# Kernel tuning notes

Measured on AMD Instinct MI355X. Metric: run time of the kernel, lower is better.

The kernel has to match this reference:

```python
import jax, jax.numpy as jnp
import numpy as np

GROUP1 = jnp.array([2, 3, 5, 6, 1, 4, 0, 7, 8, 9, 14, 15, 11, 12, 10, 13])
GROUP2 = jnp.array([0, 1, 2, 3, 5, 6, 4, 7])
NUM_HEADS = 8
LN_EPS = 1e-5


def setup_inputs() -> dict:
    key = jax.random.key(0)
    ks = jax.random.split(key, 4)
    B, N, C = 4096, 16, 512
    s = 1.0 / np.sqrt(C)
    return {
        "x": jax.random.normal(ks[0], (B, N, C), dtype=jnp.float32),
        "Wq": jax.random.normal(ks[1], (C, C), dtype=jnp.float32) * s,
        "Wkv": jax.random.normal(ks[2], (C, 2 * C), dtype=jnp.float32) * s,
        "Wproj": jax.random.normal(ks[3], (C, C), dtype=jnp.float32) * s,
        "bproj": jnp.zeros((C,), dtype=jnp.float32),
        "gamma": jnp.ones((C,), dtype=jnp.float32),
        "beta": jnp.zeros((C,), dtype=jnp.float32),
    }


def reference(x, Wq, Wkv, Wproj, bproj, gamma, beta):
    B, N, C = x.shape
    H = NUM_HEADS
    hd = C // H
    scale = hd ** -0.5

    # gather into fixed groups, avg-pool adjacent pairs along the joint axis
    p1 = x[:, GROUP1].reshape(B, 8, 2, C).mean(axis=2)   # [B, 8, C]
    p2 = x[:, GROUP2].reshape(B, 4, 2, C).mean(axis=2)   # [B, 4, C]
    pools = jnp.concatenate([x, p1, p2], axis=1)         # [B, 28, C]

    # LayerNorm over channel dim
    mu = pools.mean(axis=-1, keepdims=True)
    var = pools.var(axis=-1, keepdims=True)
    pools = (pools - mu) * jax.lax.rsqrt(var + LN_EPS) * gamma + beta

    q = (x @ Wq).reshape(B, N, H, hd)                    # [B, N, H, hd]
    kv = (pools @ Wkv).reshape(B, -1, 2, H, hd)          # [B, 28, 2, H, hd]
    k, v = kv[:, :, 0], kv[:, :, 1]                      # [B, 28, H, hd]

    attn = jnp.einsum("bnhd,bmhd->bhnm", q, k) * scale   # [B, H, N, 28]
    attn = jax.nn.softmax(attn, axis=-1)
    out = jnp.einsum("bhnm,bmhd->bnhd", attn, v).reshape(B, N, C)
    return out @ Wproj + bproj
```

## Files before the change

### kernel.cpp

```cpp
#include <hip/hip_runtime.h>

typedef unsigned short u16;
typedef __attribute__((ext_vector_type(8))) short s8v;
typedef __attribute__((ext_vector_type(4))) float f4v;

#define NB 4

__device__ __forceinline__ float bf2f(u16 u) {
    union { unsigned u; float f; } c; c.u = ((unsigned)u) << 16; return c.f;
}
__device__ __forceinline__ u16 f2bf(float f) {
    union { float f; unsigned u; } c; c.f = f;
    return (u16)((c.u + 0x7FFFu + ((c.u >> 16) & 1u)) >> 16);
}
__device__ __forceinline__ f4v mfma16(s8v a, s8v b, f4v c) {
    return __builtin_amdgcn_mfma_f32_16x16x32_bf16(a, b, c, 0, 0, 0);
}

__constant__ int POOL_A[12] = {2,5,1,0,8,14,11,10, 0,2,5,4};
__constant__ int POOL_B[12] = {3,6,4,7,9,15,12,13, 1,3,6,7};

__global__ void pack_wcat(const float* __restrict__ Wq, const float* __restrict__ Wkv,
                          const float* __restrict__ gamma, u16* __restrict__ Wfrag) {
    int blk = blockIdx.x;
    int kt = blk & 15, hn = blk >> 4;
    int nt = hn % 12, h = hn / 12;
    int lane = threadIdx.x, l15 = lane & 15, quad = lane >> 4;
    int r0 = kt * 32 + quad * 8;
    s8v v;
    if (nt < 4) {
        int c = h * 64 + nt * 16 + l15;
#pragma unroll
        for (int j = 0; j < 8; ++j) v[j] = (short)f2bf(Wq[(size_t)(r0 + j) * 512 + c]);
    } else {
        int c = (nt < 8) ? (h * 64 + (nt - 4) * 16 + l15)
                         : (512 + h * 64 + (nt - 8) * 16 + l15);
#pragma unroll
        for (int j = 0; j < 8; ++j)
            v[j] = (short)f2bf(gamma[r0 + j] * Wkv[(size_t)(r0 + j) * 1024 + c]);
    }
    *(s8v*)&Wfrag[(size_t)blk * 512 + lane * 8] = v;
}

__global__ void pack_wp(const float* __restrict__ Wproj, u16* __restrict__ Wpfrag) {
    int blk = blockIdx.x;
    int n = blk & 31, hk = blk >> 5;
    int kt = hk & 1, h = hk >> 1;
    int lane = threadIdx.x, l15 = lane & 15, quad = lane >> 4;
    int r0 = h * 64 + kt * 32 + quad * 8;
    int c = n * 16 + l15;
    s8v v;
#pragma unroll
    for (int j = 0; j < 8; ++j) v[j] = (short)f2bf(Wproj[(size_t)(r0 + j) * 512 + c]);
    *(s8v*)&Wpfrag[(size_t)blk * 512 + lane * 8] = v;
}

__global__ void gemv_g(const float* __restrict__ Wkv, const float* __restrict__ gamma,
                       const float* __restrict__ beta, float* __restrict__ gkv) {
    __shared__ float red[256];
    int o = blockIdx.x * 64 + (threadIdx.x & 63);
    int rc = threadIdx.x >> 6;
    int h = o >> 8, s = (o >> 6) & 3, c = o & 63;
    int col = (s < 2) ? (h * 64 + c) : (512 + h * 64 + c);
    const float* vec = (s & 1) ? beta : gamma;
    float acc = 0.f;
    for (int r = rc * 128; r < rc * 128 + 128; ++r)
        acc += vec[r] * Wkv[(size_t)r * 1024 + col];
    red[threadIdx.x] = acc;
    __syncthreads();
    if (rc == 0)
        gkv[o] = red[threadIdx.x] + red[threadIdx.x + 64] +
                 red[threadIdx.x + 128] + red[threadIdx.x + 192];
}

__global__ __launch_bounds__(1024, 4) void fused_spa(
    const float* __restrict__ x,
    const u16*  __restrict__ Wfrag,
    const u16*  __restrict__ Wpfrag,
    const float* __restrict__ gkv,
    const float* __restrict__ bproj,
    float* __restrict__ out)
{
    __shared__ __align__(16) unsigned char smem[162816];
    u16*   XS   = (u16*)smem;
    float* YS   = (float*)(smem + 66560);
    u16*   QH   = (u16*)(smem + 100352);
    u16*   OS   = (u16*)(smem + 109568);
    u16*   KH   = (u16*)(smem + 118784);
    u16*   VT   = (u16*)(smem + 137216);
    u16*   PB   = (u16*)(smem + 157696);
    float* STraw   = (float*)(smem + 161792);
    float* STcross = (float*)(smem + 162304);
    float* STfin   = (float*)(smem + 161792);

    const int tid  = (int)threadIdx.x;
    const int w    = tid >> 6;
    const int lane = tid & 63;
    const int l15  = lane & 15;
    const int quad = lane >> 4;
    const size_t grow0 = (size_t)blockIdx.x * (NB * 16);
    const int abatch = w - 12;

    {
        int row = tid >> 4, col = (tid & 15) * 32;
        const float4* src = (const float4*)(x + (grow0 + row) * 512 + col);
        u16* dst = XS + row * 520 + col;
#pragma unroll
        for (int i = 0; i < 4; ++i) {
            float4 f0 = src[2 * i], f1 = src[2 * i + 1];
            s8v o;
            o[0] = (short)f2bf(f0.x); o[1] = (short)f2bf(f0.y);
            o[2] = (short)f2bf(f0.z); o[3] = (short)f2bf(f0.w);
            o[4] = (short)f2bf(f1.x); o[5] = (short)f2bf(f1.y);
            o[6] = (short)f2bf(f1.z); o[7] = (short)f2bf(f1.w);
            *(s8v*)(dst + i * 8) = o;
        }
    }
    __syncthreads();

    {
#pragma unroll
        for (int i = 0; i < 4; ++i) {
            int row = w * 4 + i;
            s8v t = *(const s8v*)&XS[row * 520 + lane * 8];
            float s = 0.f, s2 = 0.f;
#pragma unroll
            for (int j = 0; j < 8; ++j) { float v = bf2f((u16)t[j]); s += v; s2 += v * v; }
#pragma unroll
            for (int d = 1; d < 64; d <<= 1) { s += __shfl_xor(s, d); s2 += __shfl_xor(s2, d); }
            if (lane == 0) { STraw[row * 2] = s * (1.f/512.f); STraw[row * 2 + 1] = s2 * (1.f/512.f); }
        }
#pragma unroll
        for (int i = 0; i < 3; ++i) {
            int d = w * 3 + i;
            int batch = d / 12, pr = d % 12;
            int ra = batch * 16 + POOL_A[pr], rb = batch * 16 + POOL_B[pr];
            s8v ta = *(const s8v*)&XS[ra * 520 + lane * 8];
            s8v tb = *(const s8v*)&XS[rb * 520 + lane * 8];
            float s = 0.f;
#pragma unroll
            for (int j = 0; j < 8; ++j) s += bf2f((u16)ta[j]) * bf2f((u16)tb[j]);
#pragma unroll
            for (int dd = 1; dd < 64; dd <<= 1) s += __shfl_xor(s, dd);
            if (lane == 0) STcross[batch * 12 + pr] = s * (1.f/512.f);
        }
    }
    __syncthreads();

    {
        float f_rstd = 0.f, f_nmu = 0.f;
        if (tid < 112) {
            int batch = tid / 28, pr = tid % 28;
            float mu, E2;
            if (pr < 16) {
                mu = STraw[(batch * 16 + pr) * 2];
                E2 = STraw[(batch * 16 + pr) * 2 + 1];
            } else {
                int j = pr - 16;
                int ra = batch * 16 + POOL_A[j], rb = batch * 16 + POOL_B[j];
                float ma = STraw[ra * 2], mb = STraw[rb * 2];
                float Ea = STraw[ra * 2 + 1], Eb = STraw[rb * 2 + 1];
                mu = 0.5f * (ma + mb);
                E2 = 0.25f * (Ea + 2.f * STcross[batch * 12 + j] + Eb);
            }
            float var = E2 - mu * mu;
            f_rstd = rsqrtf(var + 1e-5f);
            f_nmu  = -f_rstd * mu;
        }
        __syncthreads();
        if (tid < 112) { STfin[tid * 2] = f_rstd; STfin[tid * 2 + 1] = f_nmu; }
        __syncthreads();
    }

    f4v psum[8] = {};
    s8v aq0 = {}, aq1 = {};

    for (int h = 0; h <= 8; ++h) {
        if (h < 8 && w < 12) {
            f4v acc[4] = {};
            const u16* bp = Wfrag + ((size_t)(h * 12 + w) * 16) * 512 + lane * 8;
            for (int kt = 0; kt < 16; ++kt) {
                s8v bb = *(const s8v*)(bp + kt * 512);
                int ka = kt * 32 + quad * 8;
#pragma unroll
                for (int m = 0; m < 4; ++m) {
                    s8v a = *(const s8v*)&XS[(m * 16 + l15) * 520 + ka];
                    acc[m] = mfma16(a, bb, acc[m]);
                }
            }
            if (w < 4) {
#pragma unroll
                for (int m = 0; m < 4; ++m)
#pragma unroll
                    for (int r = 0; r < 4; ++r)
                        QH[(m * 16 + quad * 4 + r) * 72 + w * 16 + l15] = f2bf(acc[m][r] * 0.125f);
            } else if (w < 8) {
#pragma unroll
                for (int m = 0; m < 4; ++m)
#pragma unroll
                    for (int r = 0; r < 4; ++r)
                        YS[(m * 16 + quad * 4 + r) * 132 + (w - 4) * 16 + l15] = acc[m][r];
            } else {
#pragma unroll
                for (int m = 0; m < 4; ++m)
#pragma unroll
                    for (int r = 0; r < 4; ++r)
                        YS[(m * 16 + quad * 4 + r) * 132 + 64 + (w - 8) * 16 + l15] = acc[m][r];
            }
        } else if (h >= 1 && w >= 12) {
            f4v s0 = {}, s1 = {};
            {
                s8v bk0 = *(const s8v*)&KH[(abatch * 32 + l15) * 72 + quad * 8];
                s8v bk1 = *(const s8v*)&KH[(abatch * 32 + 16 + l15) * 72 + quad * 8];
                s0 = mfma16(aq0, bk0, s0);
                s1 = mfma16(aq0, bk1, s1);
                bk0 = *(const s8v*)&KH[(abatch * 32 + l15) * 72 + 32 + quad * 8];
                bk1 = *(const s8v*)&KH[(abatch * 32 + 16 + l15) * 72 + 32 + quad * 8];
                s0 = mfma16(aq1, bk0, s0);
                s1 = mfma16(aq1, bk1, s1);
            }
            bool valid1 = (l15 < 12);
#pragma unroll
            for (int r = 0; r < 4; ++r) {
                float v0 = s0[r];
                float v1 = valid1 ? s1[r] : -1e30f;
                float mx = fmaxf(v0, v1);
#pragma unroll
                for (int d = 1; d < 16; d <<= 1) mx = fmaxf(mx, __shfl_xor(mx, d));
                float p0 = __expf(v0 - mx);
                float p1 = valid1 ? __expf(v1 - mx) : 0.f;
                float sm = p0 + p1;
#pragma unroll
                for (int d = 1; d < 16; d <<= 1) sm += __shfl_xor(sm, d);
                float inv = 1.f / sm;
                int row = quad * 4 + r;
                PB[(abatch * 16 + row) * 32 + l15]      = f2bf(p0 * inv);
                PB[(abatch * 16 + row) * 32 + 16 + l15] = f2bf(p1 * inv);
            }
            s8v ap = *(const s8v*)&PB[(abatch * 16 + l15) * 32 + quad * 8];
#pragma unroll
            for (int nt = 0; nt < 4; ++nt) {
                s8v bv = *(const s8v*)&VT[(abatch * 64 + nt * 16 + l15) * 40 + quad * 8];
                f4v o = {};
                o = mfma16(ap, bv, o);
#pragma unroll
                for (int r = 0; r < 4; ++r)
                    OS[(abatch * 16 + quad * 4 + r) * 72 + nt * 16 + l15] = f2bf(o[r]);
            }
        }
        __syncthreads();

        if (h >= 1) {
            const int hp = h - 1;
#pragma unroll
            for (int kt = 0; kt < 2; ++kt) {
                int ka = kt * 32 + quad * 8;
                s8v a[4];
#pragma unroll
                for (int m = 0; m < 4; ++m)
                    a[m] = *(const s8v*)&OS[(m * 16 + l15) * 72 + ka];
#pragma unroll
                for (int nn = 0; nn < 2; ++nn) {
                    int n = w * 2 + nn;
                    s8v bb = *(const s8v*)&Wpfrag[((size_t)((hp * 2 + kt) * 32 + n)) * 512 + lane * 8];
#pragma unroll
                    for (int m = 0; m < 4; ++m)
                        psum[m * 2 + nn] = mfma16(a[m], bb, psum[m * 2 + nn]);
                }
            }
        }
        if (h < 8) {
            {
                int rowid = tid >> 3;
                int c0 = (tid & 7) * 8;
                int batch = rowid >> 5, pr = rowid & 31;
                if (pr < 28) {
                    float alpha = STfin[(batch * 28 + pr) * 2];
                    float beta_ = STfin[(batch * 28 + pr) * 2 + 1];
                    float yk[8], yv[8];
                    if (pr < 16) {
                        const float* yr = YS + (batch * 16 + pr) * 132;
#pragma unroll
                        for (int i = 0; i < 8; ++i) { yk[i] = yr[c0 + i]; yv[i] = yr[64 + c0 + i]; }
                    } else {
                        int j = pr - 16;
                        const float* ya = YS + (batch * 16 + POOL_A[j]) * 132;
                        const float* yb = YS + (batch * 16 + POOL_B[j]) * 132;
#pragma unroll
                        for (int i = 0; i < 8; ++i) {
                            yk[i] = 0.5f * (ya[c0 + i] + yb[c0 + i]);
                            yv[i] = 0.5f * (ya[64 + c0 + i] + yb[64 + c0 + i]);
                        }
                    }
                    const float* g = gkv + h * 256;
                    s8v kk;
#pragma unroll
                    for (int i = 0; i < 8; ++i) {
                        float kf = alpha * yk[i] + beta_ * g[c0 + i]       + g[64 + c0 + i];
                        float vf = alpha * yv[i] + beta_ * g[128 + c0 + i] + g[192 + c0 + i];
                        kk[i] = (short)f2bf(kf);
                        VT[(batch * 64 + c0 + i) * 40 + pr] = f2bf(vf);
                    }
                    *(s8v*)&KH[(batch * 32 + pr) * 72 + c0] = kk;
                } else {
                    s8v z = {0,0,0,0,0,0,0,0};
                    *(s8v*)&KH[(batch * 32 + pr) * 72 + c0] = z;
#pragma unroll
                    for (int i = 0; i < 8; ++i) VT[(batch * 64 + c0 + i) * 40 + pr] = 0;
                }
            }
            if (w >= 12) {
                aq0 = *(const s8v*)&QH[(abatch * 16 + l15) * 72 + quad * 8];
                aq1 = *(const s8v*)&QH[(abatch * 16 + l15) * 72 + 32 + quad * 8];
            }
        }
        __syncthreads();
    }

#pragma unroll
    for (int nn = 0; nn < 2; ++nn) {
        int n = w * 2 + nn;
        float bias = bproj[n * 16 + l15];
#pragma unroll
        for (int m = 0; m < 4; ++m)
#pragma unroll
            for (int r = 0; r < 4; ++r)
                out[(grow0 + m * 16 + quad * 4 + r) * 512 + n * 16 + l15] =
                    psum[m * 2 + nn][r] + bias;
    }
}

extern "C" void kernel_launch(void* const* d_in, const int* in_sizes, int n_in,
                              void* d_out, int out_size, void* d_ws, size_t ws_size,
                              hipStream_t stream) {
    const float* x     = (const float*)d_in[0];
    const float* Wq    = (const float*)d_in[1];
    const float* Wkv   = (const float*)d_in[2];
    const float* Wproj = (const float*)d_in[3];
    const float* bproj = (const float*)d_in[4];
    const float* gamma = (const float*)d_in[5];
    const float* beta  = (const float*)d_in[6];
    float* out = (float*)d_out;

    u16*   Wfrag  = (u16*)d_ws;
    u16*   Wpfrag = Wfrag + (size_t)1536 * 512;
    float* gkv    = (float*)(Wpfrag + (size_t)512 * 512);

    pack_wcat<<<1536, 64, 0, stream>>>(Wq, Wkv, gamma, Wfrag);
    pack_wp<<<512, 64, 0, stream>>>(Wproj, Wpfrag);
    gemv_g<<<32, 256, 0, stream>>>(Wkv, gamma, beta, gkv);

    fused_spa<<<4096 / NB, 1024, 0, stream>>>(x, Wfrag, Wpfrag, gkv, bproj, out);
}
```

Baseline: 585.1 us.

## Double N-tiles per warp in QKV GEMM and vectorize V-transpose writes

Halves the number of warps doing the per-head projection GEMM (6 instead of 12), with each warp computing two output tiles so every A fragment loaded from LDS feeds two MFMAs. The V transpose store is rewritten so each lane builds 8 consecutive positions and writes one 16-byte vector, replacing scattered 2-byte transposed stores. The PB row stride is padded from 32 to 40 to reduce LDS bank conflicts, and the stats region moves to make room. The trade-off is fewer warps active during the GEMM phase, which may lengthen that phase while the idle warps wait at barriers.

```diff
diff --git a/kernel.cpp b/kernel.cpp
--- a/kernel.cpp
+++ b/kernel.cpp
@@ -81,7 +81,7 @@
     const float* __restrict__ bproj,
     float* __restrict__ out)
 {
-    __shared__ __align__(16) unsigned char smem[162816];
+    __shared__ __align__(16) unsigned char smem[163712];
     u16*   XS   = (u16*)smem;
     float* YS   = (float*)(smem + 66560);
     u16*   QH   = (u16*)(smem + 100352);
@@ -89,9 +89,9 @@
     u16*   KH   = (u16*)(smem + 118784);
     u16*   VT   = (u16*)(smem + 137216);
     u16*   PB   = (u16*)(smem + 157696);
-    float* STraw   = (float*)(smem + 161792);
-    float* STcross = (float*)(smem + 162304);
-    float* STfin   = (float*)(smem + 161792);
+    float* STraw   = (float*)(smem + 162816);
+    float* STcross = (float*)(smem + 163328);
+    float* STfin   = (float*)(smem + 162816);
 
     const int tid  = (int)threadIdx.x;
     const int w    = tid >> 6;
@@ -176,36 +176,43 @@
     s8v aq0 = {}, aq1 = {};
 
     for (int h = 0; h <= 8; ++h) {
-        if (h < 8 && w < 12) {
-            f4v acc[4] = {};
-            const u16* bp = Wfrag + ((size_t)(h * 12 + w) * 16) * 512 + lane * 8;
+        if (h < 8 && w < 6) {
+            int nt0 = (w < 4) ? w : (8 + (w - 4) * 2);
+            int nt1 = (w < 4) ? (4 + w) : (9 + (w - 4) * 2);
+            f4v acc0[4] = {}, acc1[4] = {};
+            const u16* bp0 = Wfrag + ((size_t)(h * 12 + nt0) * 16) * 512 + lane * 8;
+            const u16* bp1 = Wfrag + ((size_t)(h * 12 + nt1) * 16) * 512 + lane * 8;
+#pragma unroll 4
             for (int kt = 0; kt < 16; ++kt) {
-                s8v bb = *(const s8v*)(bp + kt * 512);
+                s8v b0 = *(const s8v*)(bp0 + kt * 512);
+                s8v b1 = *(const s8v*)(bp1 + kt * 512);
                 int ka = kt * 32 + quad * 8;
 #pragma unroll
                 for (int m = 0; m < 4; ++m) {
                     s8v a = *(const s8v*)&XS[(m * 16 + l15) * 520 + ka];
-                    acc[m] = mfma16(a, bb, acc[m]);
+                    acc0[m] = mfma16(a, b0, acc0[m]);
+                    acc1[m] = mfma16(a, b1, acc1[m]);
                 }
             }
             if (w < 4) {
 #pragma unroll
                 for (int m = 0; m < 4; ++m)
 #pragma unroll
-                    for (int r = 0; r < 4; ++r)
-                        QH[(m * 16 + quad * 4 + r) * 72 + w * 16 + l15] = f2bf(acc[m][r] * 0.125f);
-            } else if (w < 8) {
+                    for (int r = 0; r < 4; ++r) {
+                        int row = m * 16 + quad * 4 + r;
+                        QH[row * 72 + w * 16 + l15] = f2bf(acc0[m][r] * 0.125f);
+                        YS[row * 132 + w * 16 + l15] = acc1[m][r];
+                    }
+            } else {
+                int v0 = (w - 4) * 2;
 #pragma unroll
                 for (int m = 0; m < 4; ++m)
 #pragma unroll
-                    for (int r = 0; r < 4; ++r)
-                        YS[(m * 16 + quad * 4 + r) * 132 + (w - 4) * 16 + l15] = acc[m][r];
-            } else {
-#pragma unroll
-                for (int m = 0; m < 4; ++m)
-#pragma unroll
-                    for (int r = 0; r < 4; ++r)
-                        YS[(m * 16 + quad * 4 + r) * 132 + 64 + (w - 8) * 16 + l15] = acc[m][r];
+                    for (int r = 0; r < 4; ++r) {
+                        int row = m * 16 + quad * 4 + r;
+                        YS[row * 132 + 64 + v0 * 16 + l15]       = acc0[m][r];
+                        YS[row * 132 + 64 + (v0 + 1) * 16 + l15] = acc1[m][r];
+                    }
             }
         } else if (h >= 1 && w >= 12) {
             f4v s0 = {}, s1 = {};
@@ -234,10 +241,10 @@
                 for (int d = 1; d < 16; d <<= 1) sm += __shfl_xor(sm, d);
                 float inv = 1.f / sm;
                 int row = quad * 4 + r;
-                PB[(abatch * 16 + row) * 32 + l15]      = f2bf(p0 * inv);
-                PB[(abatch * 16 + row) * 32 + 16 + l15] = f2bf(p1 * inv);
-            }
-            s8v ap = *(const s8v*)&PB[(abatch * 16 + l15) * 32 + quad * 8];
+                PB[(abatch * 16 + row) * 40 + l15]      = f2bf(p0 * inv);
+                PB[(abatch * 16 + row) * 40 + 16 + l15] = f2bf(p1 * inv);
+            }
+            s8v ap = *(const s8v*)&PB[(abatch * 16 + l15) * 40 + quad * 8];
 #pragma unroll
             for (int nt = 0; nt < 4; ++nt) {
                 s8v bv = *(const s8v*)&VT[(abatch * 64 + nt * 16 + l15) * 40 + quad * 8];
@@ -277,37 +284,57 @@
                 if (pr < 28) {
                     float alpha = STfin[(batch * 28 + pr) * 2];
                     float beta_ = STfin[(batch * 28 + pr) * 2 + 1];
-                    float yk[8], yv[8];
+                    float yk[8];
                     if (pr < 16) {
                         const float* yr = YS + (batch * 16 + pr) * 132;
 #pragma unroll
-                        for (int i = 0; i < 8; ++i) { yk[i] = yr[c0 + i]; yv[i] = yr[64 + c0 + i]; }
+                        for (int i = 0; i < 8; ++i) yk[i] = yr[c0 + i];
                     } else {
                         int j = pr - 16;
                         const float* ya = YS + (batch * 16 + POOL_A[j]) * 132;
                         const float* yb = YS + (batch * 16 + POOL_B[j]) * 132;
 #pragma unroll
-                        for (int i = 0; i < 8; ++i) {
-                            yk[i] = 0.5f * (ya[c0 + i] + yb[c0 + i]);
-                            yv[i] = 0.5f * (ya[64 + c0 + i] + yb[64 + c0 + i]);
-                        }
+                        for (int i = 0; i < 8; ++i) yk[i] = 0.5f * (ya[c0 + i] + yb[c0 + i]);
                     }
                     const float* g = gkv + h * 256;
                     s8v kk;
 #pragma unroll
-                    for (int i = 0; i < 8; ++i) {
-                        float kf = alpha * yk[i] + beta_ * g[c0 + i]       + g[64 + c0 + i];
-                        float vf = alpha * yv[i] + beta_ * g[128 + c0 + i] + g[192 + c0 + i];
-                        kk[i] = (short)f2bf(kf);
-                        VT[(batch * 64 + c0 + i) * 40 + pr] = f2bf(vf);
-                    }
+                    for (int i = 0; i < 8; ++i)
+                        kk[i] = (short)f2bf(alpha * yk[i] + beta_ * g[c0 + i] + g[64 + c0 + i]);
                     *(s8v*)&KH[(batch * 32 + pr) * 72 + c0] = kk;
                 } else {
                     s8v z = {0,0,0,0,0,0,0,0};
                     *(s8v*)&KH[(batch * 32 + pr) * 72 + c0] = z;
-#pragma unroll
-                    for (int i = 0; i < 8; ++i) VT[(batch * 64 + c0 + i) * 40 + pr] = 0;
                 }
+            }
+            {
+                int vb = w >> 2, ch = w & 3;
+                int d = lane;
+                const float* g = gkv + h * 256;
+                float g2 = g[128 + d], g3 = g[192 + d];
+                s8v vv;
+#pragma unroll
+                for (int i = 0; i < 8; ++i) {
+                    int pr = ch * 8 + i;
+                    float vf;
+                    if (pr < 16) {
+                        float alpha = STfin[(vb * 28 + pr) * 2];
+                        float beta_ = STfin[(vb * 28 + pr) * 2 + 1];
+                        float yv = YS[(vb * 16 + pr) * 132 + 64 + d];
+                        vf = alpha * yv + beta_ * g2 + g3;
+                    } else if (pr < 28) {
+                        int j = pr - 16;
+                        float alpha = STfin[(vb * 28 + pr) * 2];
+                        float beta_ = STfin[(vb * 28 + pr) * 2 + 1];
+                        float yv = 0.5f * (YS[(vb * 16 + POOL_A[j]) * 132 + 64 + d] +
+                                           YS[(vb * 16 + POOL_B[j]) * 132 + 64 + d]);
+                        vf = alpha * yv + beta_ * g2 + g3;
+                    } else {
+                        vf = 0.f;
+                    }
+                    vv[i] = (short)f2bf(vf);
+                }
+                *(s8v*)&VT[((size_t)vb * 64 + d) * 40 + ch * 8] = vv;
             }
             if (w >= 12) {
                 aq0 = *(const s8v*)&QH[(abatch * 16 + l15) * 72 + quad * 8];
```

Result: slower. 761.3 us (+30.1%).
